# Performance work log

Hardware: AMD Instinct MI355X
Metric: run time of the kernel (lower is better)

## Reference

```python
import jax, jax.numpy as jnp
import numpy as np

N_G, E_G = 76800, 307200   # gg: line graph over bonds
N_L, E_L = 38400, 153600   # lg: atom graph; E_L == 2*N_G
B = 64                     # number of molecules (equal-sized subgraphs)
H = 8                      # attention heads
BOND, ATOM, IN_E, FE1 = 40, 92, 10, 36


def _egat_layer(nfeats, efeats, src, dst, N, W_node, b_node, W_ni, W_nj, W_fij, attn, bias, Fn, Fe):
    # edge scores: gather + add (u_add_v) + edge proj + bias, leaky_relu
    f_edge = (nfeats @ W_ni)[src] + (nfeats @ W_nj)[dst] + efeats @ W_fij + bias
    f_out = jax.nn.leaky_relu(f_edge).reshape(-1, H, Fe)         # [E,H,Fe]
    e = jnp.einsum('ehf,hf->eh', f_out, attn)                     # [E,H]
    # edge softmax over incoming edges of each destination node
    m = jax.lax.stop_gradient(jax.ops.segment_max(e, dst, num_segments=N))
    ex = jnp.exp(e - m[dst])
    a = ex / jax.ops.segment_sum(ex, dst, num_segments=N)[dst]    # [E,H]
    h = (nfeats @ W_node + b_node).reshape(-1, H, Fn)             # [N,H,Fn]
    h_out = jax.ops.segment_sum(h[src] * a[:, :, None], dst, num_segments=N)
    return h_out, f_out


def setup_inputs() -> dict:
    key = jax.random.key(0)
    ks = iter(jax.random.split(key, 64))
    def lin(i, o):
        return jax.random.normal(next(ks), (i, o), jnp.float32) * (1.0 / np.sqrt(i))
    inp = {}
    inp['gg_src'] = jax.random.randint(next(ks), (E_G,), 0, N_G, jnp.int32)
    inp['gg_dst'] = jnp.concatenate([jnp.arange(N_G, dtype=jnp.int32),
                                     jax.random.randint(next(ks), (E_G - N_G,), 0, N_G, jnp.int32)])
    inp['gg_nfeat'] = jax.random.normal(next(ks), (N_G, BOND), jnp.float32)
    inp['gg_efeat'] = jax.random.normal(next(ks), (E_G, IN_E), jnp.float32)
    inp['lg_src'] = jax.random.randint(next(ks), (E_L,), 0, N_L, jnp.int32)
    inp['lg_dst'] = jnp.concatenate([jnp.arange(N_L, dtype=jnp.int32),
                                     jax.random.randint(next(ks), (E_L - N_L,), 0, N_L, jnp.int32)])
    inp['lg_nfeat'] = jax.random.normal(next(ks), (N_L, ATOM), jnp.float32)
    inp['lg_efeat'] = jax.random.normal(next(ks), (E_L, BOND), jnp.float32)
    # layer1 (on gg): in_node=BOND, in_edge=IN_E, out_node=BOND, out_edge=FE1
    inp['W_node1'] = lin(BOND, H * BOND); inp['b_node1'] = jnp.zeros((H * BOND,), jnp.float32)
    inp['W_ni1'] = lin(BOND, H * FE1); inp['W_nj1'] = lin(BOND, H * FE1)
    inp['W_fij1'] = lin(IN_E, H * FE1)
    inp['attn1'] = jax.random.normal(next(ks), (H, FE1), jnp.float32) * 0.1
    inp['bias1'] = jnp.zeros((H * FE1,), jnp.float32)
    # layers 2a/2b (on lg): in_node=ATOM, in_edge=BOND, out_node=ATOM, out_edge=BOND
    for sfx in ('2a', '2b'):
        inp['W_node' + sfx] = lin(ATOM, H * ATOM); inp['b_node' + sfx] = jnp.zeros((H * ATOM,), jnp.float32)
        inp['W_ni' + sfx] = lin(ATOM, H * BOND); inp['W_nj' + sfx] = lin(ATOM, H * BOND)
        inp['W_fij' + sfx] = lin(BOND, H * BOND)
        inp['attn' + sfx] = jax.random.normal(next(ks), (H, BOND), jnp.float32) * 0.1
        inp['bias' + sfx] = jnp.zeros((H * BOND,), jnp.float32)
    # Readout: Linear(128,128) + Sigmoid + Linear(128,1) + Sigmoid
    inp['Wr1'] = lin(ATOM + FE1, 128); inp['br1'] = jnp.zeros((128,), jnp.float32)
    inp['Wr2'] = lin(128, 1); inp['br2'] = jnp.zeros((1,), jnp.float32)
    return inp


def reference(gg_src, gg_dst, gg_nfeat, gg_efeat, lg_src, lg_dst, lg_nfeat, lg_efeat,
              W_node1, b_node1, W_ni1, W_nj1, W_fij1, attn1, bias1,
              W_node2a, b_node2a, W_ni2a, W_nj2a, W_fij2a, attn2a, bias2a,
              W_node2b, b_node2b, W_ni2b, W_nj2b, W_fij2b, attn2b, bias2b,
              Wr1, br1, Wr2, br2):
    # stage 1: EGAT on gg, then sum over heads
    n1, e1 = _egat_layer(gg_nfeat, gg_efeat, gg_src, gg_dst, N_G,
                         W_node1, b_node1, W_ni1, W_nj1, W_fij1, attn1, bias1, BOND, FE1)
    y2n = n1.sum(axis=1)       # [N_G, BOND]
    y22 = e1.sum(axis=1)       # [E_G, FE1]
    # each gg-node feature repeated twice, added to lg edge features
    ef = jnp.repeat(y2n, 2, axis=0) + lg_efeat   # [E_L, BOND]
    nf = lg_nfeat
    nf, e2 = _egat_layer(nf, ef, lg_src, lg_dst, N_L,
                         W_node2a, b_node2a, W_ni2a, W_nj2a, W_fij2a, attn2a, bias2a, ATOM, BOND)
    nf = nf.sum(axis=1); ef = e2.sum(axis=1)
    nf, e2 = _egat_layer(nf, ef, lg_src, lg_dst, N_L,
                         W_node2b, b_node2b, W_ni2b, W_nj2b, W_fij2b, attn2b, bias2b, ATOM, BOND)
    nf = nf.sum(axis=1)
    # per-subgraph average pooling (equal-size subgraphs -> reshape mean).
    # NOTE: original pool_subgraphs(y_22, gg) slices an edge-indexed tensor by node
    # counts (upstream quirk); reproduced exactly by taking the first N_G rows.
    y1 = nf.reshape(B, N_L // B, ATOM).mean(axis=1)          # [B, ATOM]
    y2 = y22[:N_G].reshape(B, N_G // B, FE1).mean(axis=1)    # [B, FE1]
    y = jnp.concatenate([y1, y2], axis=1)                     # [B, 128]
    h = jax.nn.sigmoid(y @ Wr1 + br1)
    return jax.nn.sigmoid(h @ Wr2 + br2)                      # [B, 1]
```

## Files before the change

kernel.cpp:

```cpp
#include <hip/hip_runtime.h>
#include <math.h>

#define NG 76800
#define EG 307200
#define NL 38400
#define EL 153600
#define NB 64
#define NH 8

typedef __attribute__((ext_vector_type(8))) short bf16x8;
typedef __attribute__((ext_vector_type(4))) float f32x4;
typedef unsigned short u16;

__device__ __forceinline__ float sigmoidf(float x) { return 1.f / (1.f + expf(-x)); }
__device__ __forceinline__ u16 f2bf(float x) {
    unsigned u = __float_as_uint(x);
    return (u16)((u + 0x7FFFu + ((u >> 16) & 1u)) >> 16);
}
__device__ __forceinline__ float bf2f(u16 v) { return __uint_as_float(((unsigned)v) << 16); }

__global__ __launch_bounds__(256) void convert_pad_kernel(const float* __restrict__ src,
                                                          u16* __restrict__ dst,
                                                          int M, int K, int Kpad) {
    int i = blockIdx.x * 256 + threadIdx.x;
    if (i >= M * Kpad) return;
    int m = i / Kpad, k = i - m * Kpad;
    dst[i] = (k < K) ? f2bf(src[(size_t)m * K + k]) : (u16)0;
}

__global__ __launch_bounds__(256) void wtrans_kernel(const float* __restrict__ W, int ldw,
                                                     u16* __restrict__ dst,
                                                     int K, int N, int Nalloc, int Kpad) {
    int i = blockIdx.x * 256 + threadIdx.x;
    if (i >= Nalloc * Kpad) return;
    int n = i / Kpad, k = i - n * Kpad;
    dst[i] = (n < N && k < K) ? f2bf(W[(size_t)k * ldw + n]) : (u16)0;
}

__global__ __launch_bounds__(256) void wtrans_hp_kernel(const float* __restrict__ W, int ldw,
                                                        u16* __restrict__ dst,
                                                        int K, int Kpad) {
    int i = blockIdx.x * 256 + threadIdx.x;
    if (i >= 320 * Kpad) return;
    int n = i / Kpad, k = i - n * Kpad;
    int hh = n / 40, f = n - hh * 40;
    float v = (k < K && f < 36) ? W[(size_t)k * ldw + hh * 36 + f] : 0.f;
    dst[i] = f2bf(v);
}

__global__ __launch_bounds__(256) void wtrans_cat_kernel(const float* __restrict__ W, int ldw,
                                                         u16* __restrict__ dst,
                                                         int Fin, int Fout, int Nalloc, int KIN) {
    int i = blockIdx.x * 256 + threadIdx.x;
    if (i >= Nalloc * KIN) return;
    int n = i / KIN, k = i - n * KIN;
    int h = k / Fin, f = k - h * Fin;
    float v = (n < Fout) ? W[(size_t)f * ldw + h * Fout + n] : 0.f;
    dst[i] = f2bf(v);
}

__global__ __launch_bounds__(256) void bias_headsum_kernel(const float* __restrict__ b,
                                                           float* __restrict__ outp,
                                                           int Fout, int H, int Npad) {
    int i = blockIdx.x * 256 + threadIdx.x;
    if (i >= Npad) return;
    float s = 0.f;
    if (i < Fout)
        for (int h = 0; h < H; ++h) s += b[h * Fout + i];
    outp[i] = s;
}

__global__ __launch_bounds__(256) void meta_kernel(const float* __restrict__ attn1,
                                                   const float* __restrict__ bias1,
                                                   const float* __restrict__ b2a,
                                                   const float* __restrict__ b2b,
                                                   float* __restrict__ attn_p1,
                                                   float* __restrict__ bias_cat1,
                                                   float* __restrict__ bias_cat2a,
                                                   float* __restrict__ bias_cat2b) {
    int i = blockIdx.x * 256 + threadIdx.x;
    if (i < 320) {
        int hh = i / 40, f = i - hh * 40;
        attn_p1[i] = (f < 36) ? attn1[hh * 36 + f] : 0.f;
    } else if (i < 960) {
        int j = i - 320;
        float v = 0.f;
        if (j < 320) {
            int hh = j / 40, f = j - hh * 40;
            v = (f < 36) ? bias1[hh * 36 + f] : 0.f;
        }
        bias_cat1[j] = v;
    } else if (i < 1600) {
        int j = i - 960;
        bias_cat2a[j] = (j < 320) ? b2a[j] : 0.f;
    } else if (i < 2240) {
        int j = i - 1600;
        bias_cat2b[j] = (j < 320) ? b2b[j] : 0.f;
    }
}

template <int KPAD>
__global__ __launch_bounds__(256) void gemm_bf_kernel(const u16* __restrict__ A,
                                                      const u16* __restrict__ Wt,
                                                      const float* __restrict__ bias,
                                                      u16* __restrict__ C, int Ncols,
                                                      int Nstride, int ytiles) {
    __shared__ u16 st[4][16 * 72];
    const int m0 = blockIdx.x * 64;
    const int wv = threadIdx.x >> 6;
    const int lane = threadIdx.x & 63;
    const int q = lane >> 4;
    const int mr = lane & 15;
    constexpr int KS = KPAD / 32;

    const u16* Arow = A + (size_t)(m0 + wv * 16 + mr) * KPAD;
    bf16x8 af[KS];
#pragma unroll
    for (int k = 0; k < KS; ++k) af[k] = *(const bf16x8*)(Arow + k * 32 + q * 8);

    u16* myst = st[wv];
    const int rrow = lane >> 3;
    const int rcol = (lane & 7) * 8;
    const int yend = blockIdx.y * ytiles + ytiles;

    for (int yt = blockIdx.y * ytiles; yt < yend; ++yt) {
        const int n0 = yt * 64;
        f32x4 acc[4];
#pragma unroll
        for (int t = 0; t < 4; ++t) acc[t] = (f32x4){0.f, 0.f, 0.f, 0.f};
#pragma unroll
        for (int k = 0; k < KS; ++k)
#pragma unroll
            for (int t = 0; t < 4; ++t) {
                bf16x8 bv = *(const bf16x8*)(Wt + (size_t)(n0 + t * 16 + mr) * KPAD + k * 32 + q * 8);
                acc[t] = __builtin_amdgcn_mfma_f32_16x16x32_bf16(af[k], bv, acc[t], 0, 0, 0);
            }
#pragma unroll
        for (int t = 0; t < 4; ++t) {
            const int colme = n0 + t * 16 + mr;
            const float bb = (bias && colme < Ncols) ? bias[colme] : 0.f;
#pragma unroll
            for (int r = 0; r < 4; ++r)
                myst[(q * 4 + r) * 72 + t * 16 + mr] = f2bf(acc[t][r] + bb);
        }
        bf16x8 v0 = *(const bf16x8*)(myst + rrow * 72 + rcol);
        bf16x8 v1 = *(const bf16x8*)(myst + (rrow + 8) * 72 + rcol);
        const int gcol = n0 + rcol;
        if (gcol < Ncols) {
            const int grow = m0 + wv * 16 + rrow;
            *(bf16x8*)(C + (size_t)grow * Nstride + gcol) = v0;
            *(bf16x8*)(C + (size_t)(grow + 8) * Nstride + gcol) = v1;
        }
    }
}

__global__ __launch_bounds__(256) void ef2a_kernel(const float* __restrict__ lg_ef,
                                                   const u16* __restrict__ y2n,
                                                   u16* __restrict__ dst) {
    int i = blockIdx.x * 256 + threadIdx.x;
    if (i >= EL * 64) return;
    int e = i >> 6, c = i & 63;
    dst[i] = (c < 40) ? f2bf(lg_ef[(size_t)e * 40 + c] + bf2f(y2n[(size_t)(e >> 1) * 40 + c]))
                      : (u16)0;
}

template <int KPAD, int FSMODE>
__global__ __launch_bounds__(128) void pe_edge_kernel(
    const u16* __restrict__ A,
    const u16* __restrict__ Wt,
    const int* __restrict__ src, const int* __restrict__ dst,
    const u16* __restrict__ Pn,
    const float* __restrict__ attn,
    float* __restrict__ esc,
    void* __restrict__ fsum,
    int e0, int CH, int fsumE) {
    __shared__ u16 pe[16][328];
    const int wv = threadIdx.x >> 6;
    const int lane = threadIdx.x & 63;
    const int q = lane >> 4;
    const int mr = lane & 15;
    const int m0 = blockIdx.x * 16;

    {
        const int t0 = wv * 10;
        const u16* Arow = A + (size_t)(m0 + mr) * KPAD;
        f32x4 acc[10];
#pragma unroll
        for (int t = 0; t < 10; ++t) acc[t] = (f32x4){0.f, 0.f, 0.f, 0.f};
#pragma unroll
        for (int k0 = 0; k0 < KPAD; k0 += 32) {
            bf16x8 af = *(const bf16x8*)(Arow + k0 + q * 8);
#pragma unroll
            for (int t = 0; t < 10; ++t) {
                bf16x8 bv = *(const bf16x8*)(Wt + (size_t)((t0 + t) * 16 + mr) * KPAD + k0 + q * 8);
                acc[t] = __builtin_amdgcn_mfma_f32_16x16x32_bf16(af, bv, acc[t], 0, 0, 0);
            }
        }
#pragma unroll
        for (int t = 0; t < 10; ++t)
#pragma unroll
            for (int r = 0; r < 4; ++r)
                pe[q * 4 + r][(t0 + t) * 16 + mr] = f2bf(acc[t][r]);
    }
    __syncthreads();

    const int lc = (lane < 40) ? lane : 39;
    const int h = lc / 5, o = lc - h * 5;
    const int c = h * 40 + o * 8;
    const bool act = (lane < 40);

    float attn_r[8];
#pragma unroll
    for (int j = 0; j < 8; ++j) attn_r[j] = attn[c + j];

    const int row0 = wv * 8;
    int e = e0 + m0 + row0;
    int s = src[e], d = dst[e];
    bf16x8 api = *(const bf16x8*)(Pn + (size_t)s * 640 + c);
    bf16x8 apj = *(const bf16x8*)(Pn + (size_t)d * 640 + 320 + c);

#pragma unroll
    for (int ei = 0; ei < 8; ++ei) {
        bf16x8 napi, napj;
        if (ei < 7) {
            const int ne = e + 1;
            const int ns = src[ne], nd = dst[ne];
            napi = *(const bf16x8*)(Pn + (size_t)ns * 640 + c);
            napj = *(const bf16x8*)(Pn + (size_t)nd * 640 + 320 + c);
        }
        const int row = row0 + ei;
        bf16x8 ape = *(const bf16x8*)(&pe[row][c]);

        float v[8];
        float ehp = 0.f;
#pragma unroll
        for (int j = 0; j < 8; ++j) {
            float x = bf2f((u16)api[j]) + bf2f((u16)apj[j]) + bf2f((u16)ape[j]);
            x = x > 0.f ? x : 0.01f * x;
            v[j] = x;
            ehp += x * attn_r[j];
        }
        float eh = 0.f;
#pragma unroll
        for (int k = 0; k < 5; ++k) eh += __shfl(ehp, h * 5 + k, 64);
        if (act && o == 0) esc[(size_t)e * 8 + h] = eh;

        if (FSMODE != 0 && e < fsumE) {
#pragma unroll
            for (int m = 4; m >= 1; m >>= 1) {
                const int p = (h ^ m) * 5 + o;
#pragma unroll
                for (int j = 0; j < 8; ++j) v[j] += __shfl(v[j], p, 64);
            }
            if (act && h == 0) {
#pragma unroll
                for (int j = 0; j < 8; ++j) {
                    const int f = o * 8 + j;
                    if (FSMODE == 1) {
                        if (f < 36) ((float*)fsum)[(size_t)e * 36 + f] = v[j];
                    } else {
                        ((u16*)fsum)[(size_t)e * 64 + f] = f2bf(v[j]);
                    }
                }
            }
        }
        if (ei < 7) {
            api = napi;
            apj = napj;
        }
        ++e;
    }
}

__global__ __launch_bounds__(256) void hist_kernel(const int* __restrict__ dst,
                                                   int* __restrict__ cnt, int E) {
    int i = blockIdx.x * 256 + threadIdx.x;
    if (i < E) atomicAdd(&cnt[dst[i]], 1);
}

__global__ __launch_bounds__(1024) void scan_block_kernel(const int* __restrict__ cnt,
                                                          int* __restrict__ excl,
                                                          int* __restrict__ bsum, int N) {
    __shared__ int sd[1024];
    const int tid = threadIdx.x;
    const int i = blockIdx.x * 1024 + tid;
    int v = (i < N) ? cnt[i] : 0;
    sd[tid] = v;
    __syncthreads();
    for (int off = 1; off < 1024; off <<= 1) {
        int t = (tid >= off) ? sd[tid - off] : 0;
        __syncthreads();
        sd[tid] += t;
        __syncthreads();
    }
    if (i < N) excl[i] = sd[tid] - v;
    if (tid == 1023) bsum[blockIdx.x] = sd[1023];
}

__global__ void scan_top_kernel(int* __restrict__ bsum, int nblk) {
    if (threadIdx.x == 0 && blockIdx.x == 0) {
        int run = 0;
        for (int b = 0; b < nblk; ++b) {
            int t = bsum[b];
            bsum[b] = run;
            run += t;
        }
    }
}

__global__ __launch_bounds__(256) void scan_add_kernel(int* __restrict__ row_ptr,
                                                       const int* __restrict__ bsum,
                                                       int N, int E) {
    int i = blockIdx.x * 256 + threadIdx.x;
    if (i < N) row_ptr[i] += bsum[i >> 10];
    if (i == 0) row_ptr[N] = E;
}

__global__ __launch_bounds__(256) void scatter_kernel(const int* __restrict__ dst,
                                                      const int* __restrict__ src,
                                                      const int* __restrict__ row_ptr,
                                                      int* __restrict__ cur,
                                                      int* __restrict__ eidx,
                                                      int* __restrict__ srcs, int E) {
    int i = blockIdx.x * 256 + threadIdx.x;
    if (i < E) {
        int d = dst[i];
        int pos = row_ptr[d] + atomicAdd(&cur[d], 1);
        eidx[pos] = i;
        srcs[pos] = src[i];
    }
}

template <int GH>
__global__ __launch_bounds__(256) void csr_softmax_kernel(
    const int* __restrict__ row_ptr, const int* __restrict__ eidx,
    const float* __restrict__ esc, float* __restrict__ wcsr, int N) {
    constexpr int NS = 64 / GH;
    const int wid = threadIdx.x >> 6;
    const int lane = threadIdx.x & 63;
    const int nid = blockIdx.x * 4 + wid;
    if (nid >= N) return;
    const int r0 = row_ptr[nid], r1 = row_ptr[nid + 1];
    const int h = lane & (GH - 1);
    const int slot = lane / GH;

    float mx = -1e30f;
    for (int i = r0 + slot; i < r1; i += NS)
        mx = fmaxf(mx, esc[(size_t)eidx[i] * GH + h]);
#pragma unroll
    for (int m = GH; m < 64; m <<= 1) mx = fmaxf(mx, __shfl_xor(mx, m, 64));

    float den = 0.f;
    for (int i = r0 + slot; i < r1; i += NS)
        den += expf(esc[(size_t)eidx[i] * GH + h] - mx);
#pragma unroll
    for (int m = GH; m < 64; m <<= 1) den += __shfl_xor(den, m, 64);
    const float rden = 1.f / den;

    for (int i = r0 + slot; i < r1; i += NS)
        wcsr[(size_t)i * GH + h] = expf(esc[(size_t)eidx[i] * GH + h] - mx) * rden;
}

template <int Fn, int GH, int NFS, int KIN, int NOUT, int NTILES>
__global__ __launch_bounds__(256) void node_agg_gemm_kernel(
    const int* __restrict__ row_ptr,
    const int* __restrict__ srcs,
    const float* __restrict__ wcsr,
    const u16* __restrict__ nf,
    const u16* __restrict__ Wcat,
    const float* __restrict__ bsum,
    u16* __restrict__ outp,
    int N) {
    constexpr int PAIRS = Fn / 2;
    constexpr int KINP = KIN + 8;
    __shared__ u16 tile[16][KINP];
    __shared__ u16 ot[16][NTILES * 16];
    const int wv = threadIdx.x >> 6;
    const int lane = threadIdx.x & 63;
    const int q = lane >> 4;
    const int mr = lane & 15;
    const int nblk = blockIdx.x * 16;

    {
        const int col = 2 * lane;
        const bool act = (lane < PAIRS);
#pragma unroll
        for (int nn = 0; nn < 4; ++nn) {
            const int nid = nblk + wv * 4 + nn;
            const int r0 = row_ptr[nid], r1 = row_ptr[nid + 1];
            float a0[GH], a1[GH];
#pragma unroll
            for (int h = 0; h < GH; ++h) { a0[h] = 0.f; a1[h] = 0.f; }
            for (int i = r0; i < r1; i += 4) {
                const u16* prs[4];
                float wvv[4][GH];
#pragma unroll
                for (int b = 0; b < 4; ++b) {
                    const int ii = (i + b < r1) ? (i + b) : (r1 - 1);
                    prs[b] = nf + (size_t)srcs[ii] * NFS;
                    const float live = (i + b < r1) ? 1.f : 0.f;
                    const float* wp = wcsr + (size_t)ii * GH;
#pragma unroll
                    for (int h = 0; h < GH; ++h) wvv[b][h] = wp[h] * live;
                }
                if (act) {
                    unsigned pv[4];
#pragma unroll
                    for (int b = 0; b < 4; ++b) pv[b] = *(const unsigned*)(prs[b] + col);
#pragma unroll
                    for (int b = 0; b < 4; ++b) {
                        const float lo = bf2f((u16)(pv[b] & 0xFFFFu));
                        const float hi = bf2f((u16)(pv[b] >> 16));
#pragma unroll
                        for (int h = 0; h < GH; ++h) {
                            a0[h] += wvv[b][h] * lo;
                            a1[h] += wvv[b][h] * hi;
                        }
                    }
                }
            }
            if (act) {
                u16* ob = tile[wv * 4 + nn];
#pragma unroll
                for (int h = 0; h < GH; ++h) {
                    unsigned pk = (unsigned)f2bf(a0[h]) | ((unsigned)f2bf(a1[h]) << 16);
                    *(unsigned*)(ob + h * Fn + col) = pk;
                }
            }
        }
    }
    __syncthreads();

    {
        const int t0 = wv;
        const int t1 = wv + 4;
        f32x4 acc0 = (f32x4){0.f, 0.f, 0.f, 0.f};
        f32x4 acc1 = (f32x4){0.f, 0.f, 0.f, 0.f};
#pragma unroll
        for (int k0 = 0; k0 < KIN; k0 += 32) {
            bf16x8 af = *(const bf16x8*)(&tile[mr][k0 + q * 8]);
            if (t0 < NTILES) {
                bf16x8 bv = *(const bf16x8*)(Wcat + (size_t)(t0 * 16 + mr) * KIN + k0 + q * 8);
                acc0 = __builtin_amdgcn_mfma_f32_16x16x32_bf16(af, bv, acc0, 0, 0, 0);
            }
            if (t1 < NTILES) {
                bf16x8 bv = *(const bf16x8*)(Wcat + (size_t)(t1 * 16 + mr) * KIN + k0 + q * 8);
                acc1 = __builtin_amdgcn_mfma_f32_16x16x32_bf16(af, bv, acc1, 0, 0, 0);
            }
        }
        if (t0 < NTILES) {
            const float bb = bsum[t0 * 16 + mr];
#pragma unroll
            for (int r = 0; r < 4; ++r) ot[q * 4 + r][t0 * 16 + mr] = f2bf(acc0[r] + bb);
        }
        if (t1 < NTILES) {
            const float bb = bsum[t1 * 16 + mr];
#pragma unroll
            for (int r = 0; r < 4; ++r) ot[q * 4 + r][t1 * 16 + mr] = f2bf(acc1[r] + bb);
        }
    }
    __syncthreads();

    constexpr int DW = NOUT / 2;
    for (int idx = threadIdx.x; idx < 16 * DW; idx += 256) {
        const int row = idx / DW, c2 = idx - row * DW;
        unsigned pk = *(const unsigned*)(&ot[row][c2 * 2]);
        *(unsigned*)(outp + (size_t)(nblk + row) * NOUT + c2 * 2) = pk;
    }
}

__global__ __launch_bounds__(256) void readout_kernel(const u16* __restrict__ nfb,
                                                      const float* __restrict__ y22p,
                                                      const float* __restrict__ Wr1,
                                                      const float* __restrict__ br1,
                                                      const float* __restrict__ Wr2,
                                                      const float* __restrict__ br2,
                                                      float* __restrict__ out) {
    const int b = blockIdx.x;
    const int t = threadIdx.x;
    __shared__ float sA[20][96];
    __shared__ float sB[28][36];
    __shared__ float y[128];
    __shared__ float hh[128];
    __shared__ float red[128];
    if (t < 240) {
        const int cc = t % 12, rg = t / 12;
        float s[8];
#pragma unroll
        for (int j = 0; j < 8; ++j) s[j] = 0.f;
        const u16* base = nfb + (size_t)b * 600 * 96 + cc * 8;
        for (int i = rg; i < 600; i += 20) {
            bf16x8 v = *(const bf16x8*)(base + (size_t)i * 96);
#pragma unroll
            for (int j = 0; j < 8; ++j) s[j] += bf2f((u16)v[j]);
        }
#pragma unroll
        for (int j = 0; j < 8; ++j) sA[rg][cc * 8 + j] = s[j];
    }
    if (t < 252) {
        const int cc = t % 9, rg = t / 9;
        float s0 = 0.f, s1 = 0.f, s2 = 0.f, s3 = 0.f;
        const float* base = y22p + (size_t)b * 1200 * 36 + cc * 4;
        for (int i = rg; i < 1200; i += 28) {
            const float* p = base + (size_t)i * 36;
            s0 += p[0]; s1 += p[1]; s2 += p[2]; s3 += p[3];
        }
        sB[rg][cc * 4 + 0] = s0;
        sB[rg][cc * 4 + 1] = s1;
        sB[rg][cc * 4 + 2] = s2;
        sB[rg][cc * 4 + 3] = s3;
    }
    __syncthreads();
    if (t < 92) {
        float s = 0.f;
        for (int r = 0; r < 20; ++r) s += sA[r][t];
        y[t] = s * (1.f / 600.f);
    } else if (t >= 128 && t < 164) {
        const int f = t - 128;
        float s = 0.f;
        for (int r = 0; r < 28; ++r) s += sB[r][f];
        y[92 + f] = s * (1.f / 1200.f);
    }
    __syncthreads();
    if (t < 128) {
        float s = br1[t];
        for (int c = 0; c < 128; ++c) s += y[c] * Wr1[(size_t)c * 128 + t];
        hh[t] = sigmoidf(s);
    }
    __syncthreads();
    if (t < 128) red[t] = hh[t] * Wr2[t];
    __syncthreads();
    for (int k = 64; k > 0; k >>= 1) {
        if (t < k) red[t] += red[t + k];
        __syncthreads();
    }
    if (t == 0) out[b] = sigmoidf(red[0] + br2[0]);
}

static inline int cdiv(int a, int b) { return (a + b - 1) / b; }

extern "C" void kernel_launch(void* const* d_in, const int* in_sizes, int n_in,
                              void* d_out, int out_size, void* d_ws, size_t ws_size,
                              hipStream_t stream) {
    const int* gg_src = (const int*)d_in[0];
    const int* gg_dst = (const int*)d_in[1];
    const float* gg_nf = (const float*)d_in[2];
    const float* gg_ef = (const float*)d_in[3];
    const int* lg_src = (const int*)d_in[4];
    const int* lg_dst = (const int*)d_in[5];
    const float* lg_nf = (const float*)d_in[6];
    const float* lg_ef = (const float*)d_in[7];
    const float* W_node1 = (const float*)d_in[8];
    const float* b_node1 = (const float*)d_in[9];
    const float* W_ni1 = (const float*)d_in[10];
    const float* W_nj1 = (const float*)d_in[11];
    const float* W_fij1 = (const float*)d_in[12];
    const float* attn1 = (const float*)d_in[13];
    const float* bias1 = (const float*)d_in[14];
    const float* W_node2a = (const float*)d_in[15];
    const float* b_node2a = (const float*)d_in[16];
    const float* W_ni2a = (const float*)d_in[17];
    const float* W_nj2a = (const float*)d_in[18];
    const float* W_fij2a = (const float*)d_in[19];
    const float* attn2a = (const float*)d_in[20];
    const float* bias2a = (const float*)d_in[21];
    const float* W_node2b = (const float*)d_in[22];
    const float* b_node2b = (const float*)d_in[23];
    const float* W_ni2b = (const float*)d_in[24];
    const float* W_nj2b = (const float*)d_in[25];
    const float* W_fij2b = (const float*)d_in[26];
    const float* attn2b = (const float*)d_in[27];
    const float* bias2b = (const float*)d_in[28];
    const float* Wr1 = (const float*)d_in[29];
    const float* br1 = (const float*)d_in[30];
    const float* Wr2 = (const float*)d_in[31];
    const float* br2 = (const float*)d_in[32];
    float* out = (float*)d_out;

    char* ws = (char*)d_ws;
    size_t off = 0;
    auto take = [&](size_t bytes) {
        size_t o = off;
        off += (bytes + 255) & ~(size_t)255;
        return (void*)(ws + o);
    };
    u16* y2n = (u16*)take((size_t)NG * 40 * 2);
    float* y22p = (float*)take((size_t)NG * 36 * 4);
    float* esc = (float*)take((size_t)EG * 8 * 4);
    float* wcsr = (float*)take((size_t)EG * 8 * 4);
    int* gg_row = (int*)take((size_t)(NG + 1) * 4);
    int* gg_eidx = (int*)take((size_t)EG * 4);
    int* gg_srcs = (int*)take((size_t)EG * 4);
    int* gg_cnt = (int*)take((size_t)NG * 4);
    int* lg_row = (int*)take((size_t)(NL + 1) * 4);
    int* lg_eidx = (int*)take((size_t)EL * 4);
    int* lg_srcs = (int*)take((size_t)EL * 4);
    int* lg_cnt = (int*)take((size_t)NL * 4);
    int* bsum = (int*)take((size_t)128 * 4);
    u16* gg_nf_bf = (u16*)take((size_t)NG * 64 * 2);
    u16* gg_ef_bf = (u16*)take((size_t)EG * 32 * 2);
    u16* lg_nf_bf = (u16*)take((size_t)NL * 96 * 2);
    u16* nfa_bf = (u16*)take((size_t)NL * 96 * 2);
    u16* nfb_bf = (u16*)take((size_t)NL * 96 * 2);
    u16* ef_shared = (u16*)take((size_t)EL * 64 * 2);
    u16* wt_ninj1 = (u16*)take((size_t)640 * 64 * 2);
    u16* wt_fij1 = (u16*)take((size_t)320 * 32 * 2);
    u16* wt_ninj2a = (u16*)take((size_t)640 * 96 * 2);
    u16* wt_ninj2b = (u16*)take((size_t)640 * 96 * 2);
    u16* wt_fij2a = (u16*)take((size_t)320 * 64 * 2);
    u16* wt_fij2b = (u16*)take((size_t)320 * 64 * 2);
    u16* wt_cat1 = (u16*)take((size_t)64 * 320 * 2);
    u16* wt_cat2a = (u16*)take((size_t)128 * 736 * 2);
    u16* wt_cat2b = (u16*)take((size_t)128 * 736 * 2);
    float* bsum1 = (float*)take((size_t)64 * 4);
    float* bsum2a = (float*)take((size_t)128 * 4);
    float* bsum2b = (float*)take((size_t)128 * 4);
    float* attn_p1 = (float*)take((size_t)320 * 4);
    float* bias_cat1 = (float*)take((size_t)640 * 4);
    float* bias_cat2a = (float*)take((size_t)640 * 4);
    float* bias_cat2b = (float*)take((size_t)640 * 4);
    u16* slab = (u16*)take((size_t)NG * 640 * 2);

    auto cvt = [&](const float* s, u16* d, int M, int K, int Kpad) {
        convert_pad_kernel<<<cdiv(M * Kpad, 256), 256, 0, stream>>>(s, d, M, K, Kpad);
    };
    auto wtr = [&](const float* W, int ldw, u16* d, int K, int N, int Nalloc, int Kpad) {
        wtrans_kernel<<<cdiv(Nalloc * Kpad, 256), 256, 0, stream>>>(W, ldw, d, K, N, Nalloc, Kpad);
    };
    auto build_csr = [&](const int* dst, const int* src, int* row_ptr, int* eidx, int* srcs,
                         int* cnt, int N, int E) {
        hipMemsetAsync(cnt, 0, (size_t)N * 4, stream);
        hist_kernel<<<cdiv(E, 256), 256, 0, stream>>>(dst, cnt, E);
        int nblk = cdiv(N, 1024);
        scan_block_kernel<<<nblk, 1024, 0, stream>>>(cnt, row_ptr, bsum, N);
        scan_top_kernel<<<1, 64, 0, stream>>>(bsum, nblk);
        scan_add_kernel<<<cdiv(N, 256), 256, 0, stream>>>(row_ptr, bsum, N, E);
        hipMemsetAsync(cnt, 0, (size_t)N * 4, stream);
        scatter_kernel<<<cdiv(E, 256), 256, 0, stream>>>(dst, src, row_ptr, cnt, eidx, srcs, E);
    };

    build_csr(gg_dst, gg_src, gg_row, gg_eidx, gg_srcs, gg_cnt, NG, EG);
    build_csr(lg_dst, lg_src, lg_row, lg_eidx, lg_srcs, lg_cnt, NL, EL);

    cvt(gg_nf, gg_nf_bf, NG, 40, 64);
    cvt(gg_ef, gg_ef_bf, EG, 10, 32);
    cvt(lg_nf, lg_nf_bf, NL, 92, 96);
    wtrans_hp_kernel<<<cdiv(320 * 64, 256), 256, 0, stream>>>(W_ni1, 288, wt_ninj1, 40, 64);
    wtrans_hp_kernel<<<cdiv(320 * 64, 256), 256, 0, stream>>>(W_nj1, 288, wt_ninj1 + 320 * 64, 40, 64);
    wtrans_hp_kernel<<<cdiv(320 * 32, 256), 256, 0, stream>>>(W_fij1, 288, wt_fij1, 10, 32);
    wtr(W_ni2a, 320, wt_ninj2a, 92, 320, 320, 96);
    wtr(W_nj2a, 320, wt_ninj2a + 320 * 96, 92, 320, 320, 96);
    wtr(W_ni2b, 320, wt_ninj2b, 92, 320, 320, 96);
    wtr(W_nj2b, 320, wt_ninj2b + 320 * 96, 92, 320, 320, 96);
    wtr(W_fij2a, 320, wt_fij2a, 40, 320, 320, 64);
    wtr(W_fij2b, 320, wt_fij2b, 40, 320, 320, 64);
    wtrans_cat_kernel<<<cdiv(64 * 320, 256), 256, 0, stream>>>(W_node1, 320, wt_cat1, 40, 40, 64, 320);
    wtrans_cat_kernel<<<cdiv(128 * 736, 256), 256, 0, stream>>>(W_node2a, 736, wt_cat2a, 92, 92, 128, 736);
    wtrans_cat_kernel<<<cdiv(128 * 736, 256), 256, 0, stream>>>(W_node2b, 736, wt_cat2b, 92, 92, 128, 736);
    bias_headsum_kernel<<<1, 256, 0, stream>>>(b_node1, bsum1, 40, 8, 64);
    bias_headsum_kernel<<<1, 256, 0, stream>>>(b_node2a, bsum2a, 92, 8, 128);
    bias_headsum_kernel<<<1, 256, 0, stream>>>(b_node2b, bsum2b, 92, 8, 128);
    meta_kernel<<<cdiv(2240, 256), 256, 0, stream>>>(attn1, bias1, bias2a, bias2b,
                                                     attn_p1, bias_cat1, bias_cat2a, bias_cat2b);

    {
        u16* Pn1 = slab;
        gemm_bf_kernel<64><<<dim3(NG / 64, 2), 256, 0, stream>>>(
            gg_nf_bf, wt_ninj1, bias_cat1, Pn1, 640, 640, 5);
        pe_edge_kernel<32, 1><<<EG / 16, 128, 0, stream>>>(
            gg_ef_bf, wt_fij1, gg_src, gg_dst, Pn1, attn_p1, esc, y22p, 0, EG, NG);
        csr_softmax_kernel<8><<<NG / 4, 256, 0, stream>>>(gg_row, gg_eidx, esc, wcsr, NG);
        node_agg_gemm_kernel<40, 8, 64, 320, 40, 3><<<NG / 16, 256, 0, stream>>>(
            gg_row, gg_srcs, wcsr, gg_nf_bf, wt_cat1, bsum1, y2n, NG);
    }

    ef2a_kernel<<<cdiv(EL * 64, 256), 256, 0, stream>>>(lg_ef, y2n, ef_shared);

    for (int layer = 0; layer < 2; ++layer) {
        const bool a = (layer == 0);
        const u16* nf_in = a ? lg_nf_bf : nfa_bf;
        const u16* Wninj = a ? wt_ninj2a : wt_ninj2b;
        const u16* Wfij = a ? wt_fij2a : wt_fij2b;
        const u16* Wcat = a ? wt_cat2a : wt_cat2b;
        const float* bs = a ? bsum2a : bsum2b;
        const float* bcat = a ? bias_cat2a : bias_cat2b;
        const float* at = a ? attn2a : attn2b;
        u16* nf_out = a ? nfa_bf : nfb_bf;

        u16* Pn2 = slab;
        gemm_bf_kernel<96><<<dim3(NL / 64, 5), 256, 0, stream>>>(
            nf_in, Wninj, bcat, Pn2, 640, 640, 2);
        if (a)
            pe_edge_kernel<64, 2><<<EL / 16, 128, 0, stream>>>(
                ef_shared, Wfij, lg_src, lg_dst, Pn2, at, esc, ef_shared, 0, EL, EL);
        else
            pe_edge_kernel<64, 0><<<EL / 16, 128, 0, stream>>>(
                ef_shared, Wfij, lg_src, lg_dst, Pn2, at, esc, nullptr, 0, EL, 0);
        csr_softmax_kernel<8><<<NL / 4, 256, 0, stream>>>(lg_row, lg_eidx, esc, wcsr, NL);
        node_agg_gemm_kernel<92, 8, 96, 736, 96, 6><<<NL / 16, 256, 0, stream>>>(
            lg_row, lg_srcs, wcsr, nf_in, Wcat, bs, nf_out, NL);
    }

    readout_kernel<<<NB, 256, 0, stream>>>(nfb_bf, y22p, Wr1, br1, Wr2, br2, out);
}
```

Before: 897.6 us.

## Merge prep kernels, batch CSR builds, fuse edge-feature add into edge kernel

Replaces about twenty small conversion, weight-transpose and bias kernels with one index-partitioned prep kernel. The CSR builds for both graphs now share a single launch per step instead of one per graph. The lg edge-feature add (lg_ef plus repeated y2n, converted to bf16) is folded into the A-operand load of the first lg edge kernel, which drops the separate ef2a pass. The aim is to cut launch overhead and one full write/read of the padded edge-feature buffer; the cost is more branching in the prep kernel and extra zero-padding stores in the edge kernel.

```diff
diff --git a/kernel.cpp b/kernel.cpp
--- a/kernel.cpp
+++ b/kernel.cpp
@@ -19,83 +19,114 @@
 }
 __device__ __forceinline__ float bf2f(u16 v) { return __uint_as_float(((unsigned)v) << 16); }
 
-__global__ __launch_bounds__(256) void convert_pad_kernel(const float* __restrict__ src,
-                                                          u16* __restrict__ dst,
-                                                          int M, int K, int Kpad) {
-    int i = blockIdx.x * 256 + threadIdx.x;
-    if (i >= M * Kpad) return;
-    int m = i / Kpad, k = i - m * Kpad;
-    dst[i] = (k < K) ? f2bf(src[(size_t)m * K + k]) : (u16)0;
-}
-
-__global__ __launch_bounds__(256) void wtrans_kernel(const float* __restrict__ W, int ldw,
-                                                     u16* __restrict__ dst,
-                                                     int K, int N, int Nalloc, int Kpad) {
-    int i = blockIdx.x * 256 + threadIdx.x;
-    if (i >= Nalloc * Kpad) return;
-    int n = i / Kpad, k = i - n * Kpad;
-    dst[i] = (n < N && k < K) ? f2bf(W[(size_t)k * ldw + n]) : (u16)0;
-}
-
-__global__ __launch_bounds__(256) void wtrans_hp_kernel(const float* __restrict__ W, int ldw,
-                                                        u16* __restrict__ dst,
-                                                        int K, int Kpad) {
-    int i = blockIdx.x * 256 + threadIdx.x;
-    if (i >= 320 * Kpad) return;
-    int n = i / Kpad, k = i - n * Kpad;
+__device__ __forceinline__ void cvt_one(const float* src, u16* dst, int j, int K, int Kpad) {
+    int m = j / Kpad, k = j - m * Kpad;
+    dst[j] = (k < K) ? f2bf(src[(size_t)m * K + k]) : (u16)0;
+}
+__device__ __forceinline__ void wtr_one(const float* W, int ldw, u16* dst, int j, int K, int Kpad) {
+    int n = j / Kpad, k = j - n * Kpad;
+    dst[j] = (k < K) ? f2bf(W[(size_t)k * ldw + n]) : (u16)0;
+}
+__device__ __forceinline__ void whp_one(const float* W, int ldw, u16* dst, int j, int K, int Kpad) {
+    int n = j / Kpad, k = j - n * Kpad;
     int hh = n / 40, f = n - hh * 40;
     float v = (k < K && f < 36) ? W[(size_t)k * ldw + hh * 36 + f] : 0.f;
-    dst[i] = f2bf(v);
-}
-
-__global__ __launch_bounds__(256) void wtrans_cat_kernel(const float* __restrict__ W, int ldw,
-                                                         u16* __restrict__ dst,
-                                                         int Fin, int Fout, int Nalloc, int KIN) {
-    int i = blockIdx.x * 256 + threadIdx.x;
-    if (i >= Nalloc * KIN) return;
-    int n = i / KIN, k = i - n * KIN;
+    dst[j] = f2bf(v);
+}
+__device__ __forceinline__ void wcat_one(const float* W, int ldw, u16* dst, int j,
+                                         int Fin, int Fout, int KIN) {
+    int n = j / KIN, k = j - n * KIN;
     int h = k / Fin, f = k - h * Fin;
     float v = (n < Fout) ? W[(size_t)f * ldw + h * Fout + n] : 0.f;
-    dst[i] = f2bf(v);
-}
-
-__global__ __launch_bounds__(256) void bias_headsum_kernel(const float* __restrict__ b,
-                                                           float* __restrict__ outp,
-                                                           int Fout, int H, int Npad) {
+    dst[j] = f2bf(v);
+}
+__device__ __forceinline__ void bh_one(const float* b, float* outp, int j, int Fout, int H) {
+    float s = 0.f;
+    if (j < Fout)
+        for (int h = 0; h < H; ++h) s += b[h * Fout + j];
+    outp[j] = s;
+}
+
+#define P0 4915200
+#define P1 14745600
+#define P2 18432000
+#define P3 18452480
+#define P4 18472960
+#define P5 18483200
+#define P6 18513920
+#define P7 18544640
+#define P8 18575360
+#define P9 18606080
+#define P10 18626560
+#define P11 18647040
+#define P12 18667520
+#define P13 18761728
+#define P14 18855936
+#define P15 18856000
+#define P16 18856128
+#define P17 18856256
+#define P18 18858496
+
+__global__ __launch_bounds__(256) void prep_kernel(
+    const float* __restrict__ gg_nf, const float* __restrict__ gg_ef,
+    const float* __restrict__ lg_nf,
+    const float* __restrict__ W_ni1, const float* __restrict__ W_nj1,
+    const float* __restrict__ W_fij1,
+    const float* __restrict__ W_ni2a, const float* __restrict__ W_nj2a,
+    const float* __restrict__ W_ni2b, const float* __restrict__ W_nj2b,
+    const float* __restrict__ W_fij2a, const float* __restrict__ W_fij2b,
+    const float* __restrict__ W_node1, const float* __restrict__ W_node2a,
+    const float* __restrict__ W_node2b,
+    const float* __restrict__ b_node1, const float* __restrict__ b_node2a,
+    const float* __restrict__ b_node2b,
+    const float* __restrict__ attn1, const float* __restrict__ bias1,
+    const float* __restrict__ b2a, const float* __restrict__ b2b,
+    u16* __restrict__ gg_nf_bf, u16* __restrict__ gg_ef_bf, u16* __restrict__ lg_nf_bf,
+    u16* __restrict__ wt_ninj1, u16* __restrict__ wt_fij1,
+    u16* __restrict__ wt_ninj2a, u16* __restrict__ wt_ninj2b,
+    u16* __restrict__ wt_fij2a, u16* __restrict__ wt_fij2b,
+    u16* __restrict__ wt_cat1, u16* __restrict__ wt_cat2a, u16* __restrict__ wt_cat2b,
+    float* __restrict__ bsum1, float* __restrict__ bsum2a, float* __restrict__ bsum2b,
+    float* __restrict__ attn_p1, float* __restrict__ bias_cat1,
+    float* __restrict__ bias_cat2a, float* __restrict__ bias_cat2b) {
     int i = blockIdx.x * 256 + threadIdx.x;
-    if (i >= Npad) return;
-    float s = 0.f;
-    if (i < Fout)
-        for (int h = 0; h < H; ++h) s += b[h * Fout + i];
-    outp[i] = s;
-}
-
-__global__ __launch_bounds__(256) void meta_kernel(const float* __restrict__ attn1,
-                                                   const float* __restrict__ bias1,
-                                                   const float* __restrict__ b2a,
-                                                   const float* __restrict__ b2b,
-                                                   float* __restrict__ attn_p1,
-                                                   float* __restrict__ bias_cat1,
-                                                   float* __restrict__ bias_cat2a,
-                                                   float* __restrict__ bias_cat2b) {
-    int i = blockIdx.x * 256 + threadIdx.x;
-    if (i < 320) {
-        int hh = i / 40, f = i - hh * 40;
-        attn_p1[i] = (f < 36) ? attn1[hh * 36 + f] : 0.f;
-    } else if (i < 960) {
-        int j = i - 320;
-        float v = 0.f;
+    if (i >= P18) return;
+    if (i < P0) cvt_one(gg_nf, gg_nf_bf, i, 40, 64);
+    else if (i < P1) cvt_one(gg_ef, gg_ef_bf, i - P0, 10, 32);
+    else if (i < P2) cvt_one(lg_nf, lg_nf_bf, i - P1, 92, 96);
+    else if (i < P3) whp_one(W_ni1, 288, wt_ninj1, i - P2, 40, 64);
+    else if (i < P4) whp_one(W_nj1, 288, wt_ninj1 + 320 * 64, i - P3, 40, 64);
+    else if (i < P5) whp_one(W_fij1, 288, wt_fij1, i - P4, 10, 32);
+    else if (i < P6) wtr_one(W_ni2a, 320, wt_ninj2a, i - P5, 92, 96);
+    else if (i < P7) wtr_one(W_nj2a, 320, wt_ninj2a + 320 * 96, i - P6, 92, 96);
+    else if (i < P8) wtr_one(W_ni2b, 320, wt_ninj2b, i - P7, 92, 96);
+    else if (i < P9) wtr_one(W_nj2b, 320, wt_ninj2b + 320 * 96, i - P8, 92, 96);
+    else if (i < P10) wtr_one(W_fij2a, 320, wt_fij2a, i - P9, 40, 64);
+    else if (i < P11) wtr_one(W_fij2b, 320, wt_fij2b, i - P10, 40, 64);
+    else if (i < P12) wcat_one(W_node1, 320, wt_cat1, i - P11, 40, 40, 320);
+    else if (i < P13) wcat_one(W_node2a, 736, wt_cat2a, i - P12, 92, 92, 736);
+    else if (i < P14) wcat_one(W_node2b, 736, wt_cat2b, i - P13, 92, 92, 736);
+    else if (i < P15) bh_one(b_node1, bsum1, i - P14, 40, 8);
+    else if (i < P16) bh_one(b_node2a, bsum2a, i - P15, 92, 8);
+    else if (i < P17) bh_one(b_node2b, bsum2b, i - P16, 92, 8);
+    else {
+        int j = i - P17;
         if (j < 320) {
             int hh = j / 40, f = j - hh * 40;
-            v = (f < 36) ? bias1[hh * 36 + f] : 0.f;
-        }
-        bias_cat1[j] = v;
-    } else if (i < 1600) {
-        int j = i - 960;
-        bias_cat2a[j] = (j < 320) ? b2a[j] : 0.f;
-    } else if (i < 2240) {
-        int j = i - 1600;
-        bias_cat2b[j] = (j < 320) ? b2b[j] : 0.f;
+            attn_p1[j] = (f < 36) ? attn1[hh * 36 + f] : 0.f;
+        } else if (j < 960) {
+            int m = j - 320;
+            int hh = m / 40, f = m - hh * 40;
+            bias_cat1[m] = (m < 320 && f < 36) ? bias1[hh * 36 + f]
+                                               : ((m < 320) ? 0.f : 0.f);
+            if (m >= 320) bias_cat1[m] = 0.f;
+        } else if (j < 1600) {
+            int m = j - 960;
+            bias_cat2a[m] = (m < 320) ? b2a[m] : 0.f;
+        } else {
+            int m = j - 1600;
+            bias_cat2b[m] = (m < 320) ? b2b[m] : 0.f;
+        }
     }
 }
 
@@ -154,17 +185,7 @@
     }
 }
 
-__global__ __launch_bounds__(256) void ef2a_kernel(const float* __restrict__ lg_ef,
-                                                   const u16* __restrict__ y2n,
-                                                   u16* __restrict__ dst) {
-    int i = blockIdx.x * 256 + threadIdx.x;
-    if (i >= EL * 64) return;
-    int e = i >> 6, c = i & 63;
-    dst[i] = (c < 40) ? f2bf(lg_ef[(size_t)e * 40 + c] + bf2f(y2n[(size_t)(e >> 1) * 40 + c]))
-                      : (u16)0;
-}
-
-template <int KPAD, int FSMODE>
+template <int KPAD, int FSMODE, int AMODE>
 __global__ __launch_bounds__(128) void pe_edge_kernel(
     const u16* __restrict__ A,
     const u16* __restrict__ Wt,
@@ -173,7 +194,10 @@
     const float* __restrict__ attn,
     float* __restrict__ esc,
     void* __restrict__ fsum,
+    const float* __restrict__ ef32,
+    const u16* __restrict__ yadd,
     int e0, int CH, int fsumE) {
+    constexpr int KS = KPAD / 32;
     __shared__ u16 pe[16][328];
     const int wv = threadIdx.x >> 6;
     const int lane = threadIdx.x & 63;
@@ -182,20 +206,51 @@
     const int m0 = blockIdx.x * 16;
 
     {
+        bf16x8 af[KS];
+        if (AMODE == 0) {
+            const u16* Arow = A + (size_t)(m0 + mr) * KPAD;
+#pragma unroll
+            for (int k = 0; k < KS; ++k) af[k] = *(const bf16x8*)(Arow + k * 32 + q * 8);
+        } else {
+            const int row = m0 + mr;
+            {
+                const float* ep = ef32 + (size_t)row * 40 + q * 8;
+                f32x4 eA = *(const f32x4*)ep;
+                f32x4 eB = *(const f32x4*)(ep + 4);
+                bf16x8 yv = *(const bf16x8*)(yadd + (size_t)(row >> 1) * 40 + q * 8);
+                bf16x8 r;
+#pragma unroll
+                for (int j = 0; j < 4; ++j) r[j] = (short)f2bf(eA[j] + bf2f((u16)yv[j]));
+#pragma unroll
+                for (int j = 4; j < 8; ++j) r[j] = (short)f2bf(eB[j - 4] + bf2f((u16)yv[j]));
+                af[0] = r;
+            }
+            {
+                bf16x8 r = (bf16x8){0, 0, 0, 0, 0, 0, 0, 0};
+                if (q == 0) {
+                    const float* ep = ef32 + (size_t)row * 40 + 32;
+                    f32x4 eA = *(const f32x4*)ep;
+                    f32x4 eB = *(const f32x4*)(ep + 4);
+                    bf16x8 yv = *(const bf16x8*)(yadd + (size_t)(row >> 1) * 40 + 32);
+#pragma unroll
+                    for (int j = 0; j < 4; ++j) r[j] = (short)f2bf(eA[j] + bf2f((u16)yv[j]));
+#pragma unroll
+                    for (int j = 4; j < 8; ++j) r[j] = (short)f2bf(eB[j - 4] + bf2f((u16)yv[j]));
+                }
+                af[1] = r;
+            }
+        }
         const int t0 = wv * 10;
-        const u16* Arow = A + (size_t)(m0 + mr) * KPAD;
         f32x4 acc[10];
 #pragma unroll
         for (int t = 0; t < 10; ++t) acc[t] = (f32x4){0.f, 0.f, 0.f, 0.f};
 #pragma unroll
-        for (int k0 = 0; k0 < KPAD; k0 += 32) {
-            bf16x8 af = *(const bf16x8*)(Arow + k0 + q * 8);
+        for (int k = 0; k < KS; ++k)
 #pragma unroll
             for (int t = 0; t < 10; ++t) {
-                bf16x8 bv = *(const bf16x8*)(Wt + (size_t)((t0 + t) * 16 + mr) * KPAD + k0 + q * 8);
-                acc[t] = __builtin_amdgcn_mfma_f32_16x16x32_bf16(af, bv, acc[t], 0, 0, 0);
-            }
-        }
+                bf16x8 bv = *(const bf16x8*)(Wt + (size_t)((t0 + t) * 16 + mr) * KPAD + k * 32 + q * 8);
+                acc[t] = __builtin_amdgcn_mfma_f32_16x16x32_bf16(af[k], bv, acc[t], 0, 0, 0);
+            }
 #pragma unroll
         for (int t = 0; t < 10; ++t)
 #pragma unroll
@@ -263,6 +318,11 @@
                     }
                 }
             }
+            if (FSMODE == 2 && act && h == 1 && o < 3) {
+#pragma unroll
+                for (int j = 0; j < 8; ++j)
+                    ((u16*)fsum)[(size_t)e * 64 + 40 + o * 8 + j] = (u16)0;
+            }
         }
         if (ei < 7) {
             api = napi;
@@ -272,18 +332,29 @@
     }
 }
 
-__global__ __launch_bounds__(256) void hist_kernel(const int* __restrict__ dst,
-                                                   int* __restrict__ cnt, int E) {
+__global__ __launch_bounds__(256) void hist2_kernel(const int* __restrict__ gdst,
+                                                    const int* __restrict__ ldst,
+                                                    int* __restrict__ gcnt,
+                                                    int* __restrict__ lcnt) {
     int i = blockIdx.x * 256 + threadIdx.x;
-    if (i < E) atomicAdd(&cnt[dst[i]], 1);
-}
-
-__global__ __launch_bounds__(1024) void scan_block_kernel(const int* __restrict__ cnt,
-                                                          int* __restrict__ excl,
-                                                          int* __restrict__ bsum, int N) {
+    if (i < EG) atomicAdd(&gcnt[gdst[i]], 1);
+    else if (i < EG + EL) atomicAdd(&lcnt[ldst[i - EG]], 1);
+}
+
+__global__ __launch_bounds__(1024) void scan_block2_kernel(const int* __restrict__ gcnt,
+                                                           const int* __restrict__ lcnt,
+                                                           int* __restrict__ grow,
+                                                           int* __restrict__ lrow,
+                                                           int* __restrict__ bsum) {
     __shared__ int sd[1024];
+    const bool isg = blockIdx.x < 75;
+    const int* cnt = isg ? gcnt : lcnt;
+    int* excl = isg ? grow : lrow;
+    const int N = isg ? NG : NL;
+    const int b = isg ? blockIdx.x : blockIdx.x - 75;
+    int* bs = bsum + (isg ? 0 : 75);
     const int tid = threadIdx.x;
-    const int i = blockIdx.x * 1024 + tid;
+    const int i = b * 1024 + tid;
     int v = (i < N) ? cnt[i] : 0;
     sd[tid] = v;
     __syncthreads();
@@ -294,40 +365,60 @@
         __syncthreads();
     }
     if (i < N) excl[i] = sd[tid] - v;
-    if (tid == 1023) bsum[blockIdx.x] = sd[1023];
-}
-
-__global__ void scan_top_kernel(int* __restrict__ bsum, int nblk) {
-    if (threadIdx.x == 0 && blockIdx.x == 0) {
+    if (tid == 1023) bs[b] = sd[1023];
+}
+
+__global__ void scan_top2_kernel(int* __restrict__ bsum) {
+    if (blockIdx.x == 0 && threadIdx.x < 2) {
+        const int b0 = (threadIdx.x == 0) ? 0 : 75;
+        const int nb = (threadIdx.x == 0) ? 75 : 38;
         int run = 0;
-        for (int b = 0; b < nblk; ++b) {
-            int t = bsum[b];
-            bsum[b] = run;
+        for (int b = 0; b < nb; ++b) {
+            int t = bsum[b0 + b];
+            bsum[b0 + b] = run;
             run += t;
         }
     }
 }
 
-__global__ __launch_bounds__(256) void scan_add_kernel(int* __restrict__ row_ptr,
-                                                       const int* __restrict__ bsum,
-                                                       int N, int E) {
+__global__ __launch_bounds__(256) void scan_add2_kernel(int* __restrict__ grow,
+                                                        int* __restrict__ lrow,
+                                                        const int* __restrict__ bsum) {
     int i = blockIdx.x * 256 + threadIdx.x;
-    if (i < N) row_ptr[i] += bsum[i >> 10];
-    if (i == 0) row_ptr[N] = E;
-}
-
-__global__ __launch_bounds__(256) void scatter_kernel(const int* __restrict__ dst,
-                                                      const int* __restrict__ src,
-                                                      const int* __restrict__ row_ptr,
-                                                      int* __restrict__ cur,
-                                                      int* __restrict__ eidx,
-                                                      int* __restrict__ srcs, int E) {
+    if (i < NG) {
+        grow[i] += bsum[i >> 10];
+        if (i == 0) grow[NG] = EG;
+    } else if (i < NG + NL) {
+        int j = i - NG;
+        lrow[j] += bsum[75 + (j >> 10)];
+        if (j == 0) lrow[NL] = EL;
+    }
+}
+
+__global__ __launch_bounds__(256) void scatter2_kernel(const int* __restrict__ gdst,
+                                                       const int* __restrict__ gsrc,
+                                                       const int* __restrict__ ldst,
+                                                       const int* __restrict__ lsrc,
+                                                       const int* __restrict__ grow,
+                                                       const int* __restrict__ lrow,
+                                                       int* __restrict__ gcur,
+                                                       int* __restrict__ lcur,
+                                                       int* __restrict__ geidx,
+                                                       int* __restrict__ gsrcs,
+                                                       int* __restrict__ leidx,
+                                                       int* __restrict__ lsrcs) {
     int i = blockIdx.x * 256 + threadIdx.x;
-    if (i < E) {
-        int d = dst[i];
-        int pos = row_ptr[d] + atomicAdd(&cur[d], 1);
-        eidx[pos] = i;
-        srcs[pos] = src[i];
+    if (i < EG) {
+        int d = gdst[i];
+        int pos = grow[d] + atomicAdd(&gcur[d], 1);
+        geidx[pos] = i;
+        gsrcs[pos] = gsrc[i];
+    } else if (i < EG + EL) {
+        int j = i - EG;
+        int d = ldst[j];
+        int pos = lrow[d] + atomicAdd(&lcur[d], 1);
+        leidx[pos] = j;
+        lsrcs[pos] = lsrc[j];
     }
 }
 
@@ -591,11 +682,12 @@
     int* gg_row = (int*)take((size_t)(NG + 1) * 4);
     int* gg_eidx = (int*)take((size_t)EG * 4);
     int* gg_srcs = (int*)take((size_t)EG * 4);
-    int* gg_cnt = (int*)take((size_t)NG * 4);
     int* lg_row = (int*)take((size_t)(NL + 1) * 4);
     int* lg_eidx = (int*)take((size_t)EL * 4);
     int* lg_srcs = (int*)take((size_t)EL * 4);
-    int* lg_cnt = (int*)take((size_t)NL * 4);
+    int* cnt_both = (int*)take((size_t)(NG + NL) * 4);
+    int* gg_cnt = cnt_both;
+    int* lg_cnt = cnt_both + NG;
     int* bsum = (int*)take((size_t)128 * 4);
     u16* gg_nf_bf = (u16*)take((size_t)NG * 64 * 2);
     u16* gg_ef_bf = (u16*)take((size_t)EG * 32 * 2);
@@ -621,60 +713,40 @@
     float* bias_cat2b = (float*)take((size_t)640 * 4);
     u16* slab = (u16*)take((size_t)NG * 640 * 2);
 
-    auto cvt = [&](const float* s, u16* d, int M, int K, int Kpad) {
-        convert_pad_kernel<<<cdiv(M * Kpad, 256), 256, 0, stream>>>(s, d, M, K, Kpad);
-    };
-    auto wtr = [&](const float* W, int ldw, u16* d, int K, int N, int Nalloc, int Kpad) {
-        wtrans_kernel<<<cdiv(Nalloc * Kpad, 256), 256, 0, stream>>>(W, ldw, d, K, N, Nalloc, Kpad);
-    };
-    auto build_csr = [&](const int* dst, const int* src, int* row_ptr, int* eidx, int* srcs,
-                         int* cnt, int N, int E) {
-        hipMemsetAsync(cnt, 0, (size_t)N * 4, stream);
-        hist_kernel<<<cdiv(E, 256), 256, 0, stream>>>(dst, cnt, E);
-        int nblk = cdiv(N, 1024);
-        scan_block_kernel<<<nblk, 1024, 0, stream>>>(cnt, row_ptr, bsum, N);
-        scan_top_kernel<<<1, 64, 0, stream>>>(bsum, nblk);
-        scan_add_kernel<<<cdiv(N, 256), 256, 0, stream>>>(row_ptr, bsum, N, E);
-        hipMemsetAsync(cnt, 0, (size_t)N * 4, stream);
-        scatter_kernel<<<cdiv(E, 256), 256, 0, stream>>>(dst, src, row_ptr, cnt, eidx, srcs, E);
-    };
-
-    build_csr(gg_dst, gg_src, gg_row, gg_eidx, gg_srcs, gg_cnt, NG, EG);
-    build_csr(lg_dst, lg_src, lg_row, lg_eidx, lg_srcs, lg_cnt, NL, EL);
-
-    cvt(gg_nf, gg_nf_bf, NG, 40, 64);
-    cvt(gg_ef, gg_ef_bf, EG, 10, 32);
-    cvt(lg_nf, lg_nf_bf, NL, 92, 96);
-    wtrans_hp_kernel<<<cdiv(320 * 64, 256), 256, 0, stream>>>(W_ni1, 288, wt_ninj1, 40, 64);
-    wtrans_hp_kernel<<<cdiv(320 * 64, 256), 256, 0, stream>>>(W_nj1, 288, wt_ninj1 + 320 * 64, 40, 64);
-    wtrans_hp_kernel<<<cdiv(320 * 32, 256), 256, 0, stream>>>(W_fij1, 288, wt_fij1, 10, 32);
-    wtr(W_ni2a, 320, wt_ninj2a, 92, 320, 320, 96);
-    wtr(W_nj2a, 320, wt_ninj2a + 320 * 96, 92, 320, 320, 96);
-    wtr(W_ni2b, 320, wt_ninj2b, 92, 320, 320, 96);
-    wtr(W_nj2b, 320, wt_ninj2b + 320 * 96, 92, 320, 320, 96);
-    wtr(W_fij2a, 320, wt_fij2a, 40, 320, 320, 64);
-    wtr(W_fij2b, 320, wt_fij2b, 40, 320, 320, 64);
-    wtrans_cat_kernel<<<cdiv(64 * 320, 256), 256, 0, stream>>>(W_node1, 320, wt_cat1, 40, 40, 64, 320);
-    wtrans_cat_kernel<<<cdiv(128 * 736, 256), 256, 0, stream>>>(W_node2a, 736, wt_cat2a, 92, 92, 128, 736);
-    wtrans_cat_kernel<<<cdiv(128 * 736, 256), 256, 0, stream>>>(W_node2b, 736, wt_cat2b, 92, 92, 128, 736);
-    bias_headsum_kernel<<<1, 256, 0, stream>>>(b_node1, bsum1, 40, 8, 64);
-    bias_headsum_kernel<<<1, 256, 0, stream>>>(b_node2a, bsum2a, 92, 8, 128);
-    bias_headsum_kernel<<<1, 256, 0, stream>>>(b_node2b, bsum2b, 92, 8, 128);
-    meta_kernel<<<cdiv(2240, 256), 256, 0, stream>>>(attn1, bias1, bias2a, bias2b,
-                                                     attn_p1, bias_cat1, bias_cat2a, bias_cat2b);
+    hipMemsetAsync(cnt_both, 0, (size_t)(NG + NL) * 4, stream);
+    hist2_kernel<<<cdiv(EG + EL, 256), 256, 0, stream>>>(gg_dst, lg_dst, gg_cnt, lg_cnt);
+    scan_block2_kernel<<<113, 1024, 0, stream>>>(gg_cnt, lg_cnt, gg_row, lg_row, bsum);
+    scan_top2_kernel<<<1, 64, 0, stream>>>(bsum);
+    scan_add2_kernel<<<cdiv(NG + NL, 256), 256, 0, stream>>>(gg_row, lg_row, bsum);
+    hipMemsetAsync(cnt_both, 0, (size_t)(NG + NL) * 4, stream);
+    scatter2_kernel<<<cdiv(EG + EL, 256), 256, 0, stream>>>(
+        gg_dst, gg_src, lg_dst, lg_src, gg_row, lg_row, gg_cnt, lg_cnt,
+        gg_eidx, gg_srcs, lg_eidx, lg_srcs);
+
+    prep_kernel<<<cdiv(P18, 256), 256, 0, stream>>>(
+        gg_nf, gg_ef, lg_nf,
+        W_ni1, W_nj1, W_fij1,
+        W_ni2a, W_nj2a, W_ni2b, W_nj2b, W_fij2a, W_fij2b,
+        W_node1, W_node2a, W_node2b,
+        b_node1, b_node2a, b_node2b,
+        attn1, bias1, bias2a, bias2b,
+        gg_nf_bf, gg_ef_bf, lg_nf_bf,
+        wt_ninj1, wt_fij1, wt_ninj2a, wt_ninj2b, wt_fij2a, wt_fij2b,
+        wt_cat1, wt_cat2a, wt_cat2b,
+        bsum1, bsum2a, bsum2b,
+        attn_p1, bias_cat1, bias_cat2a, bias_cat2b);
 
     {
         u16* Pn1 = slab;
         gemm_bf_kernel<64><<<dim3(NG / 64, 2), 256, 0, stream>>>(
             gg_nf_bf, wt_ninj1, bias_cat1, Pn1, 640, 640, 5);
-        pe_edge_kernel<32, 1><<<EG / 16, 128, 0, stream>>>(
-            gg_ef_bf, wt_fij1, gg_src, gg_dst, Pn1, attn_p1, esc, y22p, 0, EG, NG);
+        pe_edge_kernel<32, 1, 0><<<EG / 16, 128, 0, stream>>>(
+            gg_ef_bf, wt_fij1, gg_src, gg_dst, Pn1, attn_p1, esc, y22p,
+            nullptr, nullptr, 0, EG, NG);
         csr_softmax_kernel<8><<<NG / 4, 256, 0, stream>>>(gg_row, gg_eidx, esc, wcsr, NG);
         node_agg_gemm_kernel<40, 8, 64, 320, 40, 3><<<NG / 16, 256, 0, stream>>>(
             gg_row, gg_srcs, wcsr, gg_nf_bf, wt_cat1, bsum1, y2n, NG);
     }
-
-    ef2a_kernel<<<cdiv(EL * 64, 256), 256, 0, stream>>>(lg_ef, y2n, ef_shared);
 
     for (int layer = 0; layer < 2; ++layer) {
         const bool a = (layer == 0);
@@ -691,11 +763,13 @@
         gemm_bf_kernel<96><<<dim3(NL / 64, 5), 256, 0, stream>>>(
             nf_in, Wninj, bcat, Pn2, 640, 640, 2);
         if (a)
-            pe_edge_kernel<64, 2><<<EL / 16, 128, 0, stream>>>(
-                ef_shared, Wfij, lg_src, lg_dst, Pn2, at, esc, ef_shared, 0, EL, EL);
+            pe_edge_kernel<64, 2, 1><<<EL / 16, 128, 0, stream>>>(
+                nullptr, Wfij, lg_src, lg_dst, Pn2, at, esc, ef_shared,
+                lg_ef, y2n, 0, EL, EL);
         else
-            pe_edge_kernel<64, 0><<<EL / 16, 128, 0, stream>>>(
-                ef_shared, Wfij, lg_src, lg_dst, Pn2, at, esc, nullptr, 0, EL, 0);
+            pe_edge_kernel<64, 0, 0><<<EL / 16, 128, 0, stream>>>(
+                ef_shared, Wfij, lg_src, lg_dst, Pn2, at, esc, nullptr,
+                nullptr, nullptr, 0, EL, 0);
         csr_softmax_kernel<8><<<NL / 4, 256, 0, stream>>>(lg_row, lg_eidx, esc, wcsr, NL);
         node_agg_gemm_kernel<92, 8, 96, 736, 96, 6><<<NL / 16, 256, 0, stream>>>(
             lg_row, lg_srcs, wcsr, nf_in, Wcat, bs, nf_out, NL);
```

Result: faster. 824.3 us (-8.2%).
